# Kernel optimization log

Hardware: AMD Instinct MI355X
Metric: run time of the kernel (lower is better)

The kernel has to match this reference:

```python
import jax, jax.numpy as jnp
import numpy as np

N, T, P = 8192, 2048, 24  # batch of series, time steps, seasonal period


def setup_inputs() -> dict:
    key = jax.random.key(0)
    k1, k2, k3, k4, k5, k6, k7 = jax.random.split(key, 7)
    return {
        "temp": jax.random.normal(k1, (N, T), dtype=jnp.float32),
        "alpha": jax.random.uniform(k2, (1,), dtype=jnp.float32),
        "beta": jax.random.uniform(k3, (1,), dtype=jnp.float32),
        "gamma": jax.random.uniform(k4, (1,), dtype=jnp.float32),
        "L0": jax.random.normal(k5, (N,), dtype=jnp.float32),
        "b0": jax.random.normal(k6, (N,), dtype=jnp.float32),
        "S0": jax.random.normal(k7, (N, P), dtype=jnp.float32),
        "seasonp": P,
    }


def reference(temp, alpha, beta, gamma, L0, b0, S0, seasonp):
    # Holt-Winters exponential smoothing recurrence (add trend), batched over N series.
    a, bt, g = alpha[0], beta[0], gamma[0]
    Tn = temp.shape[1]
    phases = jnp.arange(1, Tn, dtype=jnp.int32) % seasonp  # i % seasonp
    xs = temp[:, 1:].T  # [T-1, N]

    def step(carry, inp):
        L, b, buf = carry          # L,b: [N]; buf: [N, P] rolling seasonal buffer
        x, ph = inp
        s_read = buf[:, ph]        # S[i % seasonp] (most recent value at this phase)
        Ln = a * (x - s_read) + (1.0 - a) * (L + b)
        bn = bt * (Ln - L) + (1.0 - bt) * b
        sn = g * (x - Ln) + (1.0 - g) * s_read
        buf = buf.at[:, ph].set(sn)
        return (Ln, bn, buf), (Ln, bn, sn)

    (_, _, _), (Ls, bs, Ss) = jax.lax.scan(step, (L0, b0, S0), (xs, phases))
    L = jnp.concatenate([L0[:, None], Ls.T], axis=1)   # [N, T]
    b = jnp.concatenate([b0[:, None], bs.T], axis=1)   # [N, T]
    S = jnp.concatenate([S0[:, 0:1], Ss.T], axis=1)    # [N, T]
    return (L + b) * S
```

## Files before the change

### kernel.cpp

```cpp
#include <hip/hip_runtime.h>


typedef float f32x4 __attribute__((ext_vector_type(4)));

#define ALOAD(DST, PTR, OFF) \
  asm volatile("global_load_dwordx4 %0, %1, off offset:" #OFF \
               : "=v"(DST) : "v"(PTR));

#define ASTORE(PTR, VAL) \
  asm volatile("global_store_dwordx4 %0, %1, off" :: "v"(PTR), "v"(VAL));

#define WAITVM(N) \
  { asm volatile("s_waitcnt vmcnt(" #N ") expcnt(0)" ::: "memory"); \
    __builtin_amdgcn_sched_barrier(0); }

__global__ __launch_bounds__(64, 1) void hw_kernel(
    const float* __restrict__ temp,
    const float* __restrict__ alpha,
    const float* __restrict__ beta,
    const float* __restrict__ gamma,
    const float* __restrict__ L0,
    const float* __restrict__ b0,
    const float* __restrict__ S0,
    float* __restrict__ out,
    int N, int T)
{
    __shared__ float ot[2][64 * 52];

    const int lane = threadIdx.x;
    const int row0 = blockIdx.x * 64;
    const int row  = row0 + lane;
    const float* xrow = temp + (size_t)row * T;

    f32x4 A0,A1,A2,A3,A4,A5,A6,A7,A8,A9,A10,A11;
    f32x4 B0,B1,B2,B3,B4,B5,B6,B7,B8,B9,B10,B11;

#define ISSUE12(Xp, P) { \
  ALOAD(Xp##0,(P),0)    ALOAD(Xp##1,(P),16)  ALOAD(Xp##2,(P),32)  \
  ALOAD(Xp##3,(P),48)   ALOAD(Xp##4,(P),64)  ALOAD(Xp##5,(P),80)  \
  ALOAD(Xp##6,(P),96)   ALOAD(Xp##7,(P),112) ALOAD(Xp##8,(P),128) \
  ALOAD(Xp##9,(P),144)  ALOAD(Xp##10,(P),160) ALOAD(Xp##11,(P),176) }
#define ISSUE8(Xp, P) { \
  ALOAD(Xp##0,(P),0)    ALOAD(Xp##1,(P),16)  ALOAD(Xp##2,(P),32)  \
  ALOAD(Xp##3,(P),48)   ALOAD(Xp##4,(P),64)  ALOAD(Xp##5,(P),80)  \
  ALOAD(Xp##6,(P),96)   ALOAD(Xp##7,(P),112) }

    ISSUE12(A, xrow)
    ISSUE12(B, xrow + 48)
    const float* vaddr = xrow + 96;

    const float a_  = alpha[0];
    const float bt  = beta[0];
    const float g_  = gamma[0];
    const float oma = 1.0f - a_;
    const float omb = 1.0f - bt;
    const float opb = 1.0f + bt;

    float buf[24];
    {
        const float* s0r = S0 + (size_t)row * 24;
        #pragma unroll
        for (int p = 0; p < 6; ++p) {
            const f32x4 v = *reinterpret_cast<const f32x4*>(s0r + 4*p);
            buf[4*p]=v.x; buf[4*p+1]=v.y; buf[4*p+2]=v.z; buf[4*p+3]=v.w;
        }
    }
    float L = L0[row];
    float c = L + b0[row];
    float og[4];

#define GSTEP(Q, E, XE) { \
    const float x_ = (XE); \
    const float s_ = buf[(4*(Q)+(E)) % 24]; \
    const float d_ = x_ - s_; \
    const float Ln = fmaf(oma, c, a_ * d_); \
    const float t1 = fmaf(omb, c, -L); \
    const float cn = fmaf(opb, Ln, t1); \
    const float sn = fmaf(g_, d_ - Ln, s_); \
    buf[(4*(Q)+(E)) % 24] = sn; \
    og[(E)] = cn * sn; \
    L = Ln; c = cn; }

#define GROUP(Q, XV, P) { \
    GSTEP(Q,0,(XV).x) GSTEP(Q,1,(XV).y) GSTEP(Q,2,(XV).z) GSTEP(Q,3,(XV).w) \
    *reinterpret_cast<f32x4*>(&ot[P][lane*52 + 4*(Q)]) = \
        (f32x4){og[0],og[1],og[2],og[3]}; }

#define WINCOMP_A(P) { GROUP(0,A0,P) GROUP(1,A1,P) GROUP(2,A2,P) GROUP(3,A3,P) \
    GROUP(4,A4,P) GROUP(5,A5,P) GROUP(6,A6,P) GROUP(7,A7,P) GROUP(8,A8,P) \
    GROUP(9,A9,P) GROUP(10,A10,P) GROUP(11,A11,P) }
#define WINCOMP_B(P) { GROUP(0,B0,P) GROUP(1,B1,P) GROUP(2,B2,P) GROUP(3,B3,P) \
    GROUP(4,B4,P) GROUP(5,B5,P) GROUP(6,B6,P) GROUP(7,B7,P) GROUP(8,B8,P) \
    GROUP(9,B9,P) GROUP(10,B10,P) GROUP(11,B11,P) }

    const int dr = lane >> 2;
    const int dc = lane & 3;
    float* obase = out + (size_t)(row0 + dr) * T + 4*dc;

#define DRAIN1(P, RG, J) { \
    const f32x4 v_ = *reinterpret_cast<const f32x4*>( \
        &ot[P][(16*(RG)+dr)*52 + 16*(J) + 4*dc]); \
    ASTORE(obase + (size_t)(16*(RG))*T + 16*(J), v_); }

#define DRAIN(P) { \
    DRAIN1(P,0,0) DRAIN1(P,0,1) DRAIN1(P,0,2) \
    DRAIN1(P,1,0) DRAIN1(P,1,1) DRAIN1(P,1,2) \
    DRAIN1(P,2,0) DRAIN1(P,2,1) DRAIN1(P,2,2) \
    DRAIN1(P,3,0) DRAIN1(P,3,1) DRAIN1(P,3,2) \
    obase += 48; }

    WAITVM(12)
    {
        og[0] = c * buf[0];
        GSTEP(0,1,A0.y) GSTEP(0,2,A0.z) GSTEP(0,3,A0.w)
        *reinterpret_cast<f32x4*>(&ot[0][lane*52]) =
            (f32x4){og[0],og[1],og[2],og[3]};
    }
    GROUP(1,A1,0)  GROUP(2,A2,0)  GROUP(3,A3,0)  GROUP(4,A4,0)
    GROUP(5,A5,0)  GROUP(6,A6,0)  GROUP(7,A7,0)  GROUP(8,A8,0)
    GROUP(9,A9,0)  GROUP(10,A10,0) GROUP(11,A11,0)

    const int pairs = (T / 48 - 2) / 2;
    for (int h = 0; h < pairs; ++h) {
        ISSUE12(A, vaddr)
        vaddr += 48;
        DRAIN(0)
        WAITVM(24)
        WINCOMP_B(1)
        ISSUE12(B, vaddr)
        vaddr += 48;
        DRAIN(1)
        WAITVM(24)
        WINCOMP_A(0)
    }

    ISSUE8(A, vaddr)
    DRAIN(0)
    WAITVM(20)
    WINCOMP_B(1)

    DRAIN(1)
    WAITVM(12)
    GROUP(0,A0,0) GROUP(1,A1,0) GROUP(2,A2,0) GROUP(3,A3,0)
    GROUP(4,A4,0) GROUP(5,A5,0) GROUP(6,A6,0) GROUP(7,A7,0)

    DRAIN1(0,0,0) DRAIN1(0,0,1)
    DRAIN1(0,1,0) DRAIN1(0,1,1)
    DRAIN1(0,2,0) DRAIN1(0,2,1)
    DRAIN1(0,3,0) DRAIN1(0,3,1)

#undef GSTEP
#undef GROUP
#undef WINCOMP_A
#undef WINCOMP_B
#undef DRAIN1
#undef DRAIN
#undef ISSUE12
#undef ISSUE8
}

extern "C" void kernel_launch(void* const* d_in, const int* in_sizes, int n_in,
                              void* d_out, int out_size, void* d_ws, size_t ws_size,
                              hipStream_t stream) {
    const float* temp  = (const float*)d_in[0];
    const float* alpha = (const float*)d_in[1];
    const float* beta  = (const float*)d_in[2];
    const float* gamma = (const float*)d_in[3];
    const float* L0    = (const float*)d_in[4];
    const float* b0    = (const float*)d_in[5];
    const float* S0    = (const float*)d_in[6];
    float* out = (float*)d_out;

    const int N = in_sizes[4];
    const int T = in_sizes[0] / N;

    const int grid = (N + 63) / 64;
    hw_kernel<<<grid, 64, 0, stream>>>(
        temp, alpha, beta, gamma, L0, b0, S0, out, N, T);
}
```

Before: 53.16 us.

## Process 16 rows per wavefront to quadruple block count

Each 64-lane block now handles only 16 series. The four lane quarters redundantly compute the same row, and only the first 16 lanes write to shared memory. The grid grows fourfold (512 blocks instead of 128), which is meant to spread the serial recurrence across more CUs on a chip with 256 CUs. Each block drains fewer stores, so the vmcnt wait thresholds are retuned and the expcnt wait is dropped. In exchange, three quarters of the ALU work per wave is redundant, and the duplicated loads rely on cache coalescing.

New measurement: 53.30 us. No clear change (+0.2%).

```diff
diff --git a/kernel.cpp b/kernel.cpp
--- a/kernel.cpp
+++ b/kernel.cpp
@@ -11,7 +11,7 @@
   asm volatile("global_store_dwordx4 %0, %1, off" :: "v"(PTR), "v"(VAL));
 
 #define WAITVM(N) \
-  { asm volatile("s_waitcnt vmcnt(" #N ") expcnt(0)" ::: "memory"); \
+  { asm volatile("s_waitcnt vmcnt(" #N ")" ::: "memory"); \
     __builtin_amdgcn_sched_barrier(0); }
 
 __global__ __launch_bounds__(64, 1) void hw_kernel(
@@ -25,24 +25,26 @@
     float* __restrict__ out,
     int N, int T)
 {
-    __shared__ float ot[2][64 * 52];
+    __shared__ float ot[2][16 * 52];
 
     const int lane = threadIdx.x;
-    const int row0 = blockIdx.x * 64;
-    const int row  = row0 + lane;
+    const int row0 = blockIdx.x * 16;
+    const int r    = lane & 15;
+    const int row  = row0 + r;
+    const bool l16 = (lane < 16);
     const float* xrow = temp + (size_t)row * T;
 
     f32x4 A0,A1,A2,A3,A4,A5,A6,A7,A8,A9,A10,A11;
     f32x4 B0,B1,B2,B3,B4,B5,B6,B7,B8,B9,B10,B11;
 
 #define ISSUE12(Xp, P) { \
-  ALOAD(Xp##0,(P),0)    ALOAD(Xp##1,(P),16)  ALOAD(Xp##2,(P),32)  \
-  ALOAD(Xp##3,(P),48)   ALOAD(Xp##4,(P),64)  ALOAD(Xp##5,(P),80)  \
-  ALOAD(Xp##6,(P),96)   ALOAD(Xp##7,(P),112) ALOAD(Xp##8,(P),128) \
+  ALOAD(Xp##0,(P),0)    ALOAD(Xp##1,(P),16)   ALOAD(Xp##2,(P),32)  \
+  ALOAD(Xp##3,(P),48)   ALOAD(Xp##4,(P),64)   ALOAD(Xp##5,(P),80)  \
+  ALOAD(Xp##6,(P),96)   ALOAD(Xp##7,(P),112)  ALOAD(Xp##8,(P),128) \
   ALOAD(Xp##9,(P),144)  ALOAD(Xp##10,(P),160) ALOAD(Xp##11,(P),176) }
 #define ISSUE8(Xp, P) { \
-  ALOAD(Xp##0,(P),0)    ALOAD(Xp##1,(P),16)  ALOAD(Xp##2,(P),32)  \
-  ALOAD(Xp##3,(P),48)   ALOAD(Xp##4,(P),64)  ALOAD(Xp##5,(P),80)  \
+  ALOAD(Xp##0,(P),0)    ALOAD(Xp##1,(P),16)   ALOAD(Xp##2,(P),32)  \
+  ALOAD(Xp##3,(P),48)   ALOAD(Xp##4,(P),64)   ALOAD(Xp##5,(P),80)  \
   ALOAD(Xp##6,(P),96)   ALOAD(Xp##7,(P),112) }
 
     ISSUE12(A, xrow)
@@ -67,7 +69,7 @@
     }
     float L = L0[row];
     float c = L + b0[row];
-    float og[4];
+    float og[4] = {0.f, 0.f, 0.f, 0.f};
 
 #define GSTEP(Q, E, XE) { \
     const float x_ = (XE); \
@@ -83,7 +85,7 @@
 
 #define GROUP(Q, XV, P) { \
     GSTEP(Q,0,(XV).x) GSTEP(Q,1,(XV).y) GSTEP(Q,2,(XV).z) GSTEP(Q,3,(XV).w) \
-    *reinterpret_cast<f32x4*>(&ot[P][lane*52 + 4*(Q)]) = \
+    if (l16) *reinterpret_cast<f32x4*>(&ot[P][r*52 + 4*(Q)]) = \
         (f32x4){og[0],og[1],og[2],og[3]}; }
 
 #define WINCOMP_A(P) { GROUP(0,A0,P) GROUP(1,A1,P) GROUP(2,A2,P) GROUP(3,A3,P) \
@@ -97,23 +99,18 @@
     const int dc = lane & 3;
     float* obase = out + (size_t)(row0 + dr) * T + 4*dc;
 
-#define DRAIN1(P, RG, J) { \
+#define DRAIN1(P, J) { \
     const f32x4 v_ = *reinterpret_cast<const f32x4*>( \
-        &ot[P][(16*(RG)+dr)*52 + 16*(J) + 4*dc]); \
-    ASTORE(obase + (size_t)(16*(RG))*T + 16*(J), v_); }
+        &ot[P][dr*52 + 16*(J) + 4*dc]); \
+    ASTORE(obase + 16*(J), v_); }
 
-#define DRAIN(P) { \
-    DRAIN1(P,0,0) DRAIN1(P,0,1) DRAIN1(P,0,2) \
-    DRAIN1(P,1,0) DRAIN1(P,1,1) DRAIN1(P,1,2) \
-    DRAIN1(P,2,0) DRAIN1(P,2,1) DRAIN1(P,2,2) \
-    DRAIN1(P,3,0) DRAIN1(P,3,1) DRAIN1(P,3,2) \
-    obase += 48; }
+#define DRAIN(P) { DRAIN1(P,0) DRAIN1(P,1) DRAIN1(P,2) obase += 48; }
 
     WAITVM(12)
     {
         og[0] = c * buf[0];
         GSTEP(0,1,A0.y) GSTEP(0,2,A0.z) GSTEP(0,3,A0.w)
-        *reinterpret_cast<f32x4*>(&ot[0][lane*52]) =
+        if (l16) *reinterpret_cast<f32x4*>(&ot[0][r*52]) =
             (f32x4){og[0],og[1],og[2],og[3]};
     }
     GROUP(1,A1,0)  GROUP(2,A2,0)  GROUP(3,A3,0)  GROUP(4,A4,0)
@@ -125,29 +122,25 @@
         ISSUE12(A, vaddr)
         vaddr += 48;
         DRAIN(0)
-        WAITVM(24)
+        WAITVM(15)
         WINCOMP_B(1)
         ISSUE12(B, vaddr)
         vaddr += 48;
         DRAIN(1)
-        WAITVM(24)
+        WAITVM(15)
         WINCOMP_A(0)
     }
 
     ISSUE8(A, vaddr)
     DRAIN(0)
-    WAITVM(20)
+    WAITVM(11)
     WINCOMP_B(1)
 
     DRAIN(1)
-    WAITVM(12)
+    WAITVM(6)
     GROUP(0,A0,0) GROUP(1,A1,0) GROUP(2,A2,0) GROUP(3,A3,0)
     GROUP(4,A4,0) GROUP(5,A5,0) GROUP(6,A6,0) GROUP(7,A7,0)
-
-    DRAIN1(0,0,0) DRAIN1(0,0,1)
-    DRAIN1(0,1,0) DRAIN1(0,1,1)
-    DRAIN1(0,2,0) DRAIN1(0,2,1)
-    DRAIN1(0,3,0) DRAIN1(0,3,1)
+    DRAIN1(0,0) DRAIN1(0,1)
 
 #undef GSTEP
 #undef GROUP
@@ -174,7 +167,7 @@
     const int N = in_sizes[4];
     const int T = in_sizes[0] / N;
 
-    const int grid = (N + 63) / 64;
+    const int grid = (N + 15) / 16;
     hw_kernel<<<grid, 64, 0, stream>>>(
         temp, alpha, beta, gamma, L0, b0, S0, out, N, T);
 }
```
